# Kernel optimization log

Hardware: AMD Instinct MI355X
Metric: run time of the kernel (lower is better)

The kernel has to match this reference:

```python
import jax, jax.numpy as jnp
import numpy as np

N_NODES = 50000
N_EDGES = 800000
D_IN = 128
D_HID = 128
D_OUT = 128


def _sage_conv(x, row, col, Wl, Wr, b):
    # PyG SAGEConv (mean aggregation, root weight, bias):
    # out = mean_{j in N(i)} x_j @ Wl^T + x_i @ Wr^T + b
    n = x.shape[0]
    msg = x[col]                                            # [E, D] gather from source nodes
    agg = jax.ops.segment_sum(msg, row, num_segments=n)     # [N, D]
    deg = jax.ops.segment_sum(jnp.ones((row.shape[0],), x.dtype), row, num_segments=n)
    agg = agg / jnp.maximum(deg, 1.0)[:, None]
    return agg @ Wl.T + x @ Wr.T + b


def setup_inputs() -> dict:
    key = jax.random.key(0)
    ks = jax.random.split(key, 12)
    x = jax.random.normal(ks[0], (N_NODES, D_IN), dtype=jnp.float32)
    edge_row = jax.random.randint(ks[1], (N_EDGES,), 0, N_NODES)
    edge_col = jax.random.randint(ks[2], (N_EDGES,), 0, N_NODES)
    dims = [(D_HID, D_IN), (D_HID, D_HID), (D_OUT, D_HID)]
    inp = {"x": x, "edge_row": edge_row, "edge_col": edge_col}
    for i, (do, di) in enumerate(dims):
        s = 1.0 / np.sqrt(di)
        inp[f"Wl{i}"] = jax.random.uniform(ks[3 + 3 * i], (do, di), jnp.float32, -s, s)
        inp[f"Wr{i}"] = jax.random.uniform(ks[4 + 3 * i], (do, di), jnp.float32, -s, s)
        inp[f"b{i}"] = jax.random.uniform(ks[5 + 3 * i], (do,), jnp.float32, -s, s)
    return inp


def reference(x, edge_row, edge_col, Wl0, Wr0, b0, Wl1, Wr1, b1, Wl2, Wr2, b2):
    # Single branch (num_layers=[3]), use_res=True, dropout=0 (eval mode).
    params = [(Wl0, Wr0, b0), (Wl1, Wr1, b1), (Wl2, Wr2, b2)]
    x1 = _sage_conv(x, edge_row, edge_col, *params[0])
    for Wl, Wr, b in params[1:]:
        x2 = x1
        x1 = jax.nn.relu(x1)
        x1 = _sage_conv(x1, edge_row, edge_col, Wl, Wr, b) + x2
    # x_final = sum(branches) / number; one branch -> divide by 1
    return x1 / 1.0
```

## Files before the change

### kernel.cpp

```cpp
#include <hip/hip_runtime.h>

#define NN 50000
#define NE 800000
#define D  128

typedef _Float16 f16;
typedef _Float16 f16x4 __attribute__((ext_vector_type(4)));
typedef _Float16 f16x8 __attribute__((ext_vector_type(8)));
typedef float f32x4 __attribute__((ext_vector_type(4)));
typedef float f32x2 __attribute__((ext_vector_type(2)));
typedef unsigned short u16;
typedef unsigned int u32;
typedef unsigned char u8;

__global__ __launch_bounds__(256) void prep(
    const float* __restrict__ x, f16* __restrict__ xf, u8* __restrict__ xf8,
    const float* w0, const float* w1, const float* w2,
    const float* w3, const float* w4, const float* w5,
    f16* d0, f16* d1, f16* d2, f16* d3, f16* d4, f16* d5,
    int* __restrict__ deg) {
    int b = blockIdx.x;
    if (b < 6250) {
        int i = b * 256 + threadIdx.x;
        float4 v = ((const float4*)x)[i];
        f16x4 o = {(f16)v.x, (f16)v.y, (f16)v.z, (f16)v.w};
        ((f16x4*)xf)[i] = o;
        u32 lo = __builtin_amdgcn_cvt_pk_fp8_f32(v.x, v.y, 0, false);
        u32 pk = __builtin_amdgcn_cvt_pk_fp8_f32(v.z, v.w, lo, true);
        ((u32*)xf8)[i] = pk;
    } else if (b < 6346) {
        int wb = b - 6250;
        int mat = wb >> 4;
        const float* s; f16* d;
        switch (mat) {
            case 0: s = w0; d = d0; break; case 1: s = w1; d = d1; break;
            case 2: s = w2; d = d2; break; case 3: s = w3; d = d3; break;
            case 4: s = w4; d = d4; break; default: s = w5; d = d5; break;
        }
        int i = (wb & 15) * 256 + threadIdx.x;
        float4 v = ((const float4*)s)[i];
        f16x4 o = {(f16)v.x, (f16)v.y, (f16)v.z, (f16)v.w};
        ((f16x4*)d)[i] = o;
    } else {
        int i = (b - 6346) * 256 + threadIdx.x;
        if (i < NN) deg[i] = 0;
    }
}


__global__ __launch_bounds__(256) void count_deg_rank(
    const int* __restrict__ row, int* __restrict__ deg, u16* __restrict__ rank, int e) {
    int i = blockIdx.x * blockDim.x + threadIdx.x;
    if (i < e) rank[i] = (u16)atomicAdd(&deg[row[i]], 1);
}

__global__ void scan_partial(const int* __restrict__ deg, int* __restrict__ bsum, int n) {
    __shared__ int s[1024];
    int i = blockIdx.x * 1024 + threadIdx.x;
    s[threadIdx.x] = (i < n) ? deg[i] : 0;
    __syncthreads();
    for (int off = 512; off > 0; off >>= 1) {
        if (threadIdx.x < off) s[threadIdx.x] += s[threadIdx.x + off];
        __syncthreads();
    }
    if (threadIdx.x == 0) bsum[blockIdx.x] = s[0];
}

__global__ void scan_final(const int* __restrict__ deg, const int* __restrict__ bsum,
                           int* __restrict__ offsets, int n, int nb) {
    __shared__ int s[1024];
    __shared__ int base;
    if (threadIdx.x < 64) {
        int t = threadIdx.x;
        int v = (t < nb && t < (int)blockIdx.x) ? bsum[t] : 0;
#pragma unroll
        for (int m = 1; m < 64; m <<= 1) v += __shfl_xor(v, m, 64);
        if (t == 0) base = v;
    }
    int i = blockIdx.x * 1024 + threadIdx.x;
    int dv = (i < n) ? deg[i] : 0;
    s[threadIdx.x] = dv;
    __syncthreads();
    for (int off = 1; off < 1024; off <<= 1) {
        int t = (threadIdx.x >= (unsigned)off) ? s[threadIdx.x - off] : 0;
        __syncthreads();
        s[threadIdx.x] += t;
        __syncthreads();
    }
    if (i < n) {
        offsets[i + 1] = s[threadIdx.x] + base;
        if (i == 0) offsets[0] = 0;
    }
}

__global__ __launch_bounds__(256) void fill_csr(
    const int* __restrict__ row, const int* __restrict__ col,
    const u16* __restrict__ rank, const int* __restrict__ offsets,
    u16* __restrict__ csr_col, int e) {
    int i = blockIdx.x * blockDim.x + threadIdx.x;
    if (i < e) {
        int p = offsets[row[i]] + (int)rank[i];
        csr_col[p] = (u16)col[i];
    }
}

__global__ __launch_bounds__(256) void aggregate_f8(
    const u8* __restrict__ h8, const int* __restrict__ offsets,
    const u16* __restrict__ csr, f16* __restrict__ agg) {
    int node = blockIdx.x * 4 + (threadIdx.x >> 6);
    int lane = threadIdx.x & 63;
    int sub = lane >> 4, fl = lane & 15;
    int s0 = offsets[node], e0 = offsets[node + 1];
    int deg = e0 - s0;

    float acc[8];
#pragma unroll
    for (int u = 0; u < 8; ++u) acc[u] = 0.f;

    const u8* hp = h8 + fl * 8;

#define UNPACK_ADD(w)                                                  \
    do {                                                               \
        f32x2 p;                                                       \
        p = __builtin_amdgcn_cvt_pk_f32_fp8((w).x, false);             \
        acc[0] += p.x; acc[1] += p.y;                                  \
        p = __builtin_amdgcn_cvt_pk_f32_fp8((w).x, true);              \
        acc[2] += p.x; acc[3] += p.y;                                  \
        p = __builtin_amdgcn_cvt_pk_f32_fp8((w).y, false);             \
        acc[4] += p.x; acc[5] += p.y;                                  \
        p = __builtin_amdgcn_cvt_pk_f32_fp8((w).y, true);              \
        acc[6] += p.x; acc[7] += p.y;                                  \
    } while (0)

    int j = s0 + sub;
    for (int it = deg >> 3; it > 0; --it, j += 8) {
        int c0 = (int)csr[j];
        int c1 = (int)csr[j + 4];
        uint2 w0 = *(const uint2*)(hp + (size_t)c0 * D);
        uint2 w1 = *(const uint2*)(hp + (size_t)c1 * D);
        UNPACK_ADD(w0);
        UNPACK_ADD(w1);
    }
    if (deg & 4) {
        int c = (int)csr[j];
        uint2 w = *(const uint2*)(hp + (size_t)c * D);
        UNPACK_ADD(w);
        j += 4;
    }
    if (sub < (deg & 3)) {
        int c = (int)csr[j];
        uint2 w = *(const uint2*)(hp + (size_t)c * D);
        UNPACK_ADD(w);
    }
#undef UNPACK_ADD

#pragma unroll
    for (int u = 0; u < 8; ++u) {
        acc[u] += __shfl_xor(acc[u], 16, 64);
        acc[u] += __shfl_xor(acc[u], 32, 64);
    }
    if (sub == 0) {
        float inv = 1.f / fmaxf((float)deg, 1.f);
        f16x8 o;
#pragma unroll
        for (int u = 0; u < 8; ++u) o[u] = (f16)(acc[u] * inv);
        *((f16x8*)(agg + (size_t)node * D) + fl) = o;
    }
}

#define WPAD 72

template<int RELU_X, int ADD_RES, int OUT_F32>
__global__ __launch_bounds__(256, 4) void sage_gemm_mfma(
    const f16* __restrict__ aggb, const f16* __restrict__ xb,
    const f16* __restrict__ Wl, const f16* __restrict__ Wr,
    const float* __restrict__ bias, float* __restrict__ outf,
    f16* __restrict__ outh, u8* __restrict__ out8) {
    __shared__ f16 sW[2][128][WPAD];

    const int tid  = threadIdx.x;
    const int wave = tid >> 6;
    const int lane = tid & 63;
    const int lm = lane & 15;
    const int q  = lane >> 4;
    const int mt = blockIdx.x * 64 + wave * 16;

    int row = mt + lm;
    int rclamp = (row < NN) ? row : NN - 1;

    f16x8 Aa[4], Ax[4];
    const f16* arow = aggb + (size_t)rclamp * D + q * 8;
    const f16* xrow = xb  + (size_t)rclamp * D + q * 8;
#pragma unroll
    for (int ks = 0; ks < 4; ++ks) {
        Aa[ks] = *(const f16x8*)(arow + ks * 32);
        f16x8 v = *(const f16x8*)(xrow + ks * 32);
        if (RELU_X) {
#pragma unroll
            for (int u = 0; u < 8; ++u) v[u] = (v[u] < (f16)0) ? (f16)0 : v[u];
        }
        Ax[ks] = v;
    }

    f32x4 acc[8];
#pragma unroll
    for (int nt = 0; nt < 8; ++nt) acc[nt] = (f32x4){0.f, 0.f, 0.f, 0.f};

    for (int p = 0; p < 2; ++p) {
        __syncthreads();
#pragma unroll
        for (int it = 0; it < 8; ++it) {
            int idx = tid + it * 256;
            int mat = idx >> 10;
            int n   = (idx >> 3) & 127;
            int c   = idx & 7;
            const f16* W = mat ? Wr : Wl;
            f16x8 v = *(const f16x8*)(W + n * D + p * 64 + c * 8);
            *(f16x8*)&sW[mat][n][c * 8] = v;
        }
        __syncthreads();

#pragma unroll
        for (int nt = 0; nt < 8; ++nt) {
#pragma unroll
            for (int k2 = 0; k2 < 2; ++k2) {
                f16x8 bl = *(const f16x8*)&sW[0][nt * 16 + lm][k2 * 32 + q * 8];
                acc[nt] = __builtin_amdgcn_mfma_f32_16x16x32_f16(Aa[p * 2 + k2], bl, acc[nt], 0, 0, 0);
                f16x8 br = *(const f16x8*)&sW[1][nt * 16 + lm][k2 * 32 + q * 8];
                acc[nt] = __builtin_amdgcn_mfma_f32_16x16x32_f16(Ax[p * 2 + k2], br, acc[nt], 0, 0, 0);
            }
        }
    }

#pragma unroll
    for (int nt = 0; nt < 8; ++nt) {
        int n = nt * 16 + lm;
        float bval = bias[n];
#pragma unroll
        for (int r = 0; r < 4; ++r) {
            int m = mt + q * 4 + r;
            if (m < NN) {
                size_t idx = (size_t)m * D + n;
                float v = acc[nt][r] + bval;
                if (ADD_RES) v += (float)xb[idx];
                if (OUT_F32) {
                    outf[idx] = v;
                } else {
                    outh[idx] = (f16)v;
                    u32 t = __builtin_amdgcn_cvt_pk_fp8_f32(fmaxf(v, 0.f), 0.f, 0, false);
                    out8[idx] = (u8)(t & 0xffu);
                }
            }
        }
    }
}


extern "C" void kernel_launch(void* const* d_in, const int* in_sizes, int n_in,
                              void* d_out, int out_size, void* d_ws, size_t ws_size,
                              hipStream_t stream) {
    const float* x    = (const float*)d_in[0];
    const int*   erow = (const int*)d_in[1];
    const int*   ecol = (const int*)d_in[2];
    const float* Wl0 = (const float*)d_in[3];
    const float* Wr0 = (const float*)d_in[4];
    const float* b0  = (const float*)d_in[5];
    const float* Wl1 = (const float*)d_in[6];
    const float* Wr1 = (const float*)d_in[7];
    const float* b1  = (const float*)d_in[8];
    const float* Wl2 = (const float*)d_in[9];
    const float* Wr2 = (const float*)d_in[10];
    const float* b2  = (const float*)d_in[11];

    char* ws = (char*)d_ws;
    size_t off = 0;
    auto carve = [&](size_t bytes) -> void* {
        void* p = ws + off;
        off = (off + bytes + 255) & ~(size_t)255;
        return p;
    };
    int*   deg     = (int*)carve((size_t)NN * 4);
    int*   offsets = (int*)carve((size_t)(NN + 1) * 4);
    int*   bsum    = (int*)carve(64 * 4);
    u16*   rank    = (u16*)carve((size_t)NE * 2);
    u16*   csr_col = (u16*)carve((size_t)NE * 2);
    f16*   xf      = (f16*)carve((size_t)NN * D * 2);
    f16*   x1      = (f16*)carve((size_t)NN * D * 2);
    f16*   aggb    = (f16*)carve((size_t)NN * D * 2);
    u8*    xf8     = (u8*)carve((size_t)NN * D);
    u8*    x1f8    = (u8*)carve((size_t)NN * D);
    f16*   wl0 = (f16*)carve(D * D * 2); f16* wr0 = (f16*)carve(D * D * 2);
    f16*   wl1 = (f16*)carve(D * D * 2); f16* wr1 = (f16*)carve(D * D * 2);
    f16*   wl2 = (f16*)carve(D * D * 2); f16* wr2 = (f16*)carve(D * D * 2);
    (void)ws_size; (void)in_sizes; (void)n_in; (void)out_size;

    float* outp = (float*)d_out;

    prep<<<6542, 256, 0, stream>>>(x, xf, xf8, Wl0, Wr0, Wl1, Wr1, Wl2, Wr2,
                                   wl0, wr0, wl1, wr1, wl2, wr2, deg);

    count_deg_rank<<<(NE + 255) / 256, 256, 0, stream>>>(erow, deg, rank, NE);
    const int nsb = (NN + 1023) / 1024;
    scan_partial<<<nsb, 1024, 0, stream>>>(deg, bsum, NN);
    scan_final<<<nsb, 1024, 0, stream>>>(deg, bsum, offsets, NN, nsb);
    fill_csr<<<(NE + 255) / 256, 256, 0, stream>>>(erow, ecol, rank, offsets, csr_col, NE);

    const int agrid = NN / 4;
    const int ggrid = (NN + 63) / 64;

    aggregate_f8<<<agrid, 256, 0, stream>>>(xf8, offsets, csr_col, aggb);
    sage_gemm_mfma<0, 0, 0><<<ggrid, 256, 0, stream>>>(aggb, xf, wl0, wr0, b0,
                                                       nullptr, x1, x1f8);
    aggregate_f8<<<agrid, 256, 0, stream>>>(x1f8, offsets, csr_col, aggb);
    sage_gemm_mfma<1, 1, 0><<<ggrid, 256, 0, stream>>>(aggb, x1, wl1, wr1, b1,
                                                       nullptr, x1, x1f8);
    aggregate_f8<<<agrid, 256, 0, stream>>>(x1f8, offsets, csr_col, aggb);
    sage_gemm_mfma<1, 1, 1><<<ggrid, 256, 0, stream>>>(aggb, x1, wl2, wr2, b2,
                                                       outp, nullptr, nullptr);
}
```

Before: 279.0 us.

## Fuse neighbor aggregation into SAGE GEMM kernel and merge scan passes

Each layer's fp8 neighbor aggregation now runs inside the MFMA GEMM kernel. A block aggregates its 64 nodes into shared memory, which is then reused for the weight tiles, so the f16 aggregate buffer no longer makes a round trip through global memory and one launch per layer is removed. The two-pass scan becomes a single kernel where each block re-sums all preceding degrees itself, and the degree/rank and CSR fill kernels now handle two edges per thread with vector loads. fp8 outputs ping-pong between two buffers, because in-place writes would race with other blocks still gathering neighbors. The risk is that the gather phase now runs at GEMM occupancy, and the GEMM cannot start until the gather finishes within each block.

```diff
diff --git a/kernel.cpp b/kernel.cpp
--- a/kernel.cpp
+++ b/kernel.cpp
@@ -49,35 +49,30 @@
 
 
 __global__ __launch_bounds__(256) void count_deg_rank(
-    const int* __restrict__ row, int* __restrict__ deg, u16* __restrict__ rank, int e) {
+    const int* __restrict__ row, int* __restrict__ deg, u16* __restrict__ rank, int e2) {
     int i = blockIdx.x * blockDim.x + threadIdx.x;
-    if (i < e) rank[i] = (u16)atomicAdd(&deg[row[i]], 1);
-}
-
-__global__ void scan_partial(const int* __restrict__ deg, int* __restrict__ bsum, int n) {
+    if (i < e2) {
+        int2 r = ((const int2*)row)[i];
+        unsigned ra = (unsigned)atomicAdd(&deg[r.x], 1);
+        unsigned rb = (unsigned)atomicAdd(&deg[r.y], 1);
+        ((unsigned*)rank)[i] = (ra & 0xffffu) | (rb << 16);
+    }
+}
+
+__global__ void scan_offsets(const int* __restrict__ deg, int* __restrict__ offsets, int n) {
     __shared__ int s[1024];
-    int i = blockIdx.x * 1024 + threadIdx.x;
-    s[threadIdx.x] = (i < n) ? deg[i] : 0;
+    int lim = blockIdx.x << 10;
+    int a = 0;
+    for (int i = threadIdx.x; i < lim; i += 1024) a += deg[i];
+    s[threadIdx.x] = a;
     __syncthreads();
     for (int off = 512; off > 0; off >>= 1) {
         if (threadIdx.x < off) s[threadIdx.x] += s[threadIdx.x + off];
         __syncthreads();
     }
-    if (threadIdx.x == 0) bsum[blockIdx.x] = s[0];
-}
-
-__global__ void scan_final(const int* __restrict__ deg, const int* __restrict__ bsum,
-                           int* __restrict__ offsets, int n, int nb) {
-    __shared__ int s[1024];
-    __shared__ int base;
-    if (threadIdx.x < 64) {
-        int t = threadIdx.x;
-        int v = (t < nb && t < (int)blockIdx.x) ? bsum[t] : 0;
-#pragma unroll
-        for (int m = 1; m < 64; m <<= 1) v += __shfl_xor(v, m, 64);
-        if (t == 0) base = v;
-    }
-    int i = blockIdx.x * 1024 + threadIdx.x;
+    int base = s[0];
+    __syncthreads();
+    int i = lim + threadIdx.x;
     int dv = (i < n) ? deg[i] : 0;
     s[threadIdx.x] = dv;
     __syncthreads();
@@ -96,28 +91,47 @@
 __global__ __launch_bounds__(256) void fill_csr(
     const int* __restrict__ row, const int* __restrict__ col,
     const u16* __restrict__ rank, const int* __restrict__ offsets,
-    u16* __restrict__ csr_col, int e) {
+    u16* __restrict__ csr_col, int e2) {
     int i = blockIdx.x * blockDim.x + threadIdx.x;
-    if (i < e) {
-        int p = offsets[row[i]] + (int)rank[i];
-        csr_col[p] = (u16)col[i];
-    }
-}
-
-__global__ __launch_bounds__(256) void aggregate_f8(
+    if (i < e2) {
+        int2 r = ((const int2*)row)[i];
+        int2 c = ((const int2*)col)[i];
+        unsigned rk = ((const unsigned*)rank)[i];
+        csr_col[offsets[r.x] + (int)(rk & 0xffffu)] = (u16)c.x;
+        csr_col[offsets[r.y] + (int)(rk >> 16)]     = (u16)c.y;
+    }
+}
+
+#define WPAD 72
+#define APAD 136
+
+template<int LAYER>
+__global__ __launch_bounds__(256, 4) void sage_fused(
     const u8* __restrict__ h8, const int* __restrict__ offsets,
-    const u16* __restrict__ csr, f16* __restrict__ agg) {
-    int node = blockIdx.x * 4 + (threadIdx.x >> 6);
-    int lane = threadIdx.x & 63;
-    int sub = lane >> 4, fl = lane & 15;
-    int s0 = offsets[node], e0 = offsets[node + 1];
-    int deg = e0 - s0;
-
-    float acc[8];
-#pragma unroll
-    for (int u = 0; u < 8; ++u) acc[u] = 0.f;
-
-    const u8* hp = h8 + fl * 8;
+    const u16* __restrict__ csr, const f16* __restrict__ xb,
+    const f16* __restrict__ Wl, const f16* __restrict__ Wr,
+    const float* __restrict__ bias, float* __restrict__ outf,
+    f16* __restrict__ outh, u8* __restrict__ out8) {
+    __shared__ __align__(16) f16 smem[2 * 128 * WPAD];
+    f16 (*aggL)[APAD] = (f16(*)[APAD])smem;
+    f16 (*sW)[128][WPAD] = (f16(*)[128][WPAD])smem;
+
+    const int tid  = threadIdx.x;
+    const int wave = tid >> 6;
+    const int lane = tid & 63;
+    const int sub = lane >> 4, fl = lane & 15;
+    const int nb0 = blockIdx.x * 64;
+
+    for (int v = wave; v < 64; v += 4) {
+        int node = nb0 + v;
+        int s0 = 0, dg = 0;
+        if (node < NN) { s0 = offsets[node]; dg = offsets[node + 1] - s0; }
+
+        float acc[8];
+#pragma unroll
+        for (int u = 0; u < 8; ++u) acc[u] = 0.f;
+
+        const u8* hp = h8 + fl * 8;
 
 #define UNPACK_ADD(w)                                                  \
     do {                                                               \
@@ -132,70 +146,56 @@
         acc[6] += p.x; acc[7] += p.y;                                  \
     } while (0)
 
-    int j = s0 + sub;
-    for (int it = deg >> 3; it > 0; --it, j += 8) {
-        int c0 = (int)csr[j];
-        int c1 = (int)csr[j + 4];
-        uint2 w0 = *(const uint2*)(hp + (size_t)c0 * D);
-        uint2 w1 = *(const uint2*)(hp + (size_t)c1 * D);
-        UNPACK_ADD(w0);
-        UNPACK_ADD(w1);
-    }
-    if (deg & 4) {
-        int c = (int)csr[j];
-        uint2 w = *(const uint2*)(hp + (size_t)c * D);
-        UNPACK_ADD(w);
-        j += 4;
-    }
-    if (sub < (deg & 3)) {
-        int c = (int)csr[j];
-        uint2 w = *(const uint2*)(hp + (size_t)c * D);
-        UNPACK_ADD(w);
-    }
+        int j = s0 + sub;
+        for (int it = dg >> 3; it > 0; --it, j += 8) {
+            int c0 = (int)csr[j];
+            int c1 = (int)csr[j + 4];
+            uint2 w0 = *(const uint2*)(hp + (size_t)c0 * D);
+            uint2 w1 = *(const uint2*)(hp + (size_t)c1 * D);
+            UNPACK_ADD(w0);
+            UNPACK_ADD(w1);
+        }
+        if (dg & 4) {
+            int c = (int)csr[j];
+            uint2 w = *(const uint2*)(hp + (size_t)c * D);
+            UNPACK_ADD(w);
+            j += 4;
+        }
+        if (sub < (dg & 3)) {
+            int c = (int)csr[j];
+            uint2 w = *(const uint2*)(hp + (size_t)c * D);
+            UNPACK_ADD(w);
+        }
 #undef UNPACK_ADD
 
 #pragma unroll
-    for (int u = 0; u < 8; ++u) {
-        acc[u] += __shfl_xor(acc[u], 16, 64);
-        acc[u] += __shfl_xor(acc[u], 32, 64);
-    }
-    if (sub == 0) {
-        float inv = 1.f / fmaxf((float)deg, 1.f);
-        f16x8 o;
-#pragma unroll
-        for (int u = 0; u < 8; ++u) o[u] = (f16)(acc[u] * inv);
-        *((f16x8*)(agg + (size_t)node * D) + fl) = o;
-    }
-}
-
-#define WPAD 72
-
-template<int RELU_X, int ADD_RES, int OUT_F32>
-__global__ __launch_bounds__(256, 4) void sage_gemm_mfma(
-    const f16* __restrict__ aggb, const f16* __restrict__ xb,
-    const f16* __restrict__ Wl, const f16* __restrict__ Wr,
-    const float* __restrict__ bias, float* __restrict__ outf,
-    f16* __restrict__ outh, u8* __restrict__ out8) {
-    __shared__ f16 sW[2][128][WPAD];
-
-    const int tid  = threadIdx.x;
-    const int wave = tid >> 6;
-    const int lane = tid & 63;
-    const int lm = lane & 15;
-    const int q  = lane >> 4;
-    const int mt = blockIdx.x * 64 + wave * 16;
-
+        for (int u = 0; u < 8; ++u) {
+            acc[u] += __shfl_xor(acc[u], 16, 64);
+            acc[u] += __shfl_xor(acc[u], 32, 64);
+        }
+        if (sub == 0) {
+            float inv = 1.f / fmaxf((float)dg, 1.f);
+            f16x8 o;
+#pragma unroll
+            for (int u = 0; u < 8; ++u) o[u] = (f16)(acc[u] * inv);
+            *(f16x8*)&aggL[v][fl * 8] = o;
+        }
+    }
+    __syncthreads();
+
+    const int lm = fl;
+    const int q  = sub;
+    const int mt = nb0 + wave * 16;
     int row = mt + lm;
     int rclamp = (row < NN) ? row : NN - 1;
 
     f16x8 Aa[4], Ax[4];
-    const f16* arow = aggb + (size_t)rclamp * D + q * 8;
-    const f16* xrow = xb  + (size_t)rclamp * D + q * 8;
+    const f16* xrow = xb + (size_t)rclamp * D + q * 8;
 #pragma unroll
     for (int ks = 0; ks < 4; ++ks) {
-        Aa[ks] = *(const f16x8*)(arow + ks * 32);
+        Aa[ks] = *(const f16x8*)&aggL[wave * 16 + lm][ks * 32 + q * 8];
         f16x8 v = *(const f16x8*)(xrow + ks * 32);
-        if (RELU_X) {
+        if (LAYER > 0) {
 #pragma unroll
             for (int u = 0; u < 8; ++u) v[u] = (v[u] < (f16)0) ? (f16)0 : v[u];
         }
@@ -242,8 +242,8 @@
             if (m < NN) {
                 size_t idx = (size_t)m * D + n;
                 float v = acc[nt][r] + bval;
-                if (ADD_RES) v += (float)xb[idx];
-                if (OUT_F32) {
+                if (LAYER > 0) v += (float)xb[idx];
+                if (LAYER == 2) {
                     outf[idx] = v;
                 } else {
                     outh[idx] = (f16)v;
@@ -281,14 +281,13 @@
     };
     int*   deg     = (int*)carve((size_t)NN * 4);
     int*   offsets = (int*)carve((size_t)(NN + 1) * 4);
-    int*   bsum    = (int*)carve(64 * 4);
     u16*   rank    = (u16*)carve((size_t)NE * 2);
     u16*   csr_col = (u16*)carve((size_t)NE * 2);
     f16*   xf      = (f16*)carve((size_t)NN * D * 2);
     f16*   x1      = (f16*)carve((size_t)NN * D * 2);
-    f16*   aggb    = (f16*)carve((size_t)NN * D * 2);
     u8*    xf8     = (u8*)carve((size_t)NN * D);
-    u8*    x1f8    = (u8*)carve((size_t)NN * D);
+    u8*    h8a     = (u8*)carve((size_t)NN * D);
+    u8*    h8b     = (u8*)carve((size_t)NN * D);
     f16*   wl0 = (f16*)carve(D * D * 2); f16* wr0 = (f16*)carve(D * D * 2);
     f16*   wl1 = (f16*)carve(D * D * 2); f16* wr1 = (f16*)carve(D * D * 2);
     f16*   wl2 = (f16*)carve(D * D * 2); f16* wr2 = (f16*)carve(D * D * 2);
@@ -299,22 +298,17 @@
     prep<<<6542, 256, 0, stream>>>(x, xf, xf8, Wl0, Wr0, Wl1, Wr1, Wl2, Wr2,
                                    wl0, wr0, wl1, wr1, wl2, wr2, deg);
 
-    count_deg_rank<<<(NE + 255) / 256, 256, 0, stream>>>(erow, deg, rank, NE);
-    const int nsb = (NN + 1023) / 1024;
-    scan_partial<<<nsb, 1024, 0, stream>>>(deg, bsum, NN);
-    scan_final<<<nsb, 1024, 0, stream>>>(deg, bsum, offsets, NN, nsb);
-    fill_csr<<<(NE + 255) / 256, 256, 0, stream>>>(erow, ecol, rank, offsets, csr_col, NE);
-
-    const int agrid = NN / 4;
+    const int e2 = NE / 2;
+    count_deg_rank<<<(e2 + 255) / 256, 256, 0, stream>>>(erow, deg, rank, e2);
+    scan_offsets<<<(NN + 1023) / 1024, 1024, 0, stream>>>(deg, offsets, NN);
+    fill_csr<<<(e2 + 255) / 256, 256, 0, stream>>>(erow, ecol, rank, offsets, csr_col, e2);
+
     const int ggrid = (NN + 63) / 64;
 
-    aggregate_f8<<<agrid, 256, 0, stream>>>(xf8, offsets, csr_col, aggb);
-    sage_gemm_mfma<0, 0, 0><<<ggrid, 256, 0, stream>>>(aggb, xf, wl0, wr0, b0,
-                                                       nullptr, x1, x1f8);
-    aggregate_f8<<<agrid, 256, 0, stream>>>(x1f8, offsets, csr_col, aggb);
-    sage_gemm_mfma<1, 1, 0><<<ggrid, 256, 0, stream>>>(aggb, x1, wl1, wr1, b1,
-                                                       nullptr, x1, x1f8);
-    aggregate_f8<<<agrid, 256, 0, stream>>>(x1f8, offsets, csr_col, aggb);
-    sage_gemm_mfma<1, 1, 1><<<ggrid, 256, 0, stream>>>(aggb, x1, wl2, wr2, b2,
-                                                       outp, nullptr, nullptr);
-}
+    sage_fused<0><<<ggrid, 256, 0, stream>>>(xf8, offsets, csr_col, xf,
+                                             wl0, wr0, b0, nullptr, x1, h8a);
+    sage_fused<1><<<ggrid, 256, 0, stream>>>(h8a, offsets, csr_col, x1,
+                                             wl1, wr1, b1, nullptr, x1, h8b);
+    sage_fused<2><<<ggrid, 256, 0, stream>>>(h8b, offsets, csr_col, x1,
+                                             wl2, wr2, b2, outp, nullptr, nullptr);
+}
```

Result: slower. 323.2 us (+15.9%).
